# Kernel optimization log

Hardware: AMD Instinct MI355X
Metric: run time of the kernel (lower is better)

Reference implementation:

```python
import jax, jax.numpy as jnp
import numpy as np

N_NODES = 8192
IN_DIM = 20000
HID = 256
LAT = 64
N_EDGES = 262144


def setup_inputs() -> dict:
    key = jax.random.key(0)
    ks = jax.random.split(key, 12)
    s_in = 1.0 / np.sqrt(IN_DIM)
    s_h = 1.0 / np.sqrt(HID)
    s_l = 1.0 / np.sqrt(LAT)
    return {
        "x": jax.random.normal(ks[0], (N_NODES, IN_DIM), jnp.float32),
        "edge_index": jax.random.randint(ks[1], (2, N_EDGES), 0, N_NODES, jnp.int64 if jax.config.jax_enable_x64 else jnp.int32),
        "w_gcn": jax.random.uniform(ks[2], (IN_DIM, HID), jnp.float32, -s_in, s_in),
        "b_gcn": jnp.zeros((HID,), jnp.float32),
        "w_enc": jax.random.uniform(ks[3], (HID, LAT), jnp.float32, -s_h, s_h),
        "b_enc": jax.random.uniform(ks[4], (LAT,), jnp.float32, -s_h, s_h),
        "w_d1": jax.random.uniform(ks[5], (LAT, HID), jnp.float32, -s_l, s_l),
        "b_d1": jax.random.uniform(ks[6], (HID,), jnp.float32, -s_l, s_l),
        "w_d2": jax.random.uniform(ks[7], (HID, IN_DIM), jnp.float32, -s_h, s_h),
        "b_d2": jax.random.uniform(ks[8], (IN_DIM,), jnp.float32, -s_h, s_h),
    }


def _gcn_conv(x, edge_index, w, b):
    """PyG GCNConv (add_self_loops=True, normalize=True): A_hat @ (x W) + b."""
    n = x.shape[0]
    h = x @ w  # [N, HID] -- project first (in_dim >> out_dim)
    loops = jnp.arange(n, dtype=edge_index.dtype)
    row = jnp.concatenate([edge_index[0], loops])  # source nodes
    col = jnp.concatenate([edge_index[1], loops])  # target nodes
    deg = jax.ops.segment_sum(jnp.ones_like(col, dtype=h.dtype), col, num_segments=n)
    dinv = jnp.where(deg > 0, jax.lax.rsqrt(deg), 0.0)
    norm = dinv[row] * dinv[col]  # [E+N]
    msg = h[row] * norm[:, None]  # gather + scale
    out = jax.ops.segment_sum(msg, col, num_segments=n)  # scatter-add
    return out + b


def reference(x, edge_index, w_gcn, b_gcn, w_enc, b_enc, w_d1, b_d1, w_d2, b_d2):
    # Encoder: GCNConv -> ReLU -> (Dropout: eval no-op) -> Linear
    h = _gcn_conv(x, edge_index, w_gcn, b_gcn)
    latent = jax.nn.relu(h) @ w_enc + b_enc  # [N, LAT]
    # Decoder: Linear -> ReLU -> (Dropout) -> Linear
    recon = jax.nn.relu(latent @ w_d1 + b_d1) @ w_d2 + b_d2  # [N, IN_DIM]
    return recon, latent
```

## Files before the change

kernel.cpp:

```cpp
#include <hip/hip_runtime.h>
#include <stdint.h>

typedef short short8 __attribute__((ext_vector_type(8)));
typedef float f32x4 __attribute__((ext_vector_type(4)));

#define N_NODES 8192
#define IN_DIM 20000
#define HIDDEN 256
#define LATENT 64
#define N_EDGES 262144
#define K_STEPS 625
#define RECON_ELEMS (8192LL * 20000LL)
#define WD2T_ROWS 20096
#define NSUB3 626

static __device__ __forceinline__ unsigned short f2bf(float f) {
  union { float f; unsigned int u; } v;
  v.f = f;
  unsigned int u = v.u;
  return (unsigned short)((u + 0x7FFFu + ((u >> 16) & 1u)) >> 16);
}

static __device__ __forceinline__ unsigned pk2bf(float a, float b) {
  return (unsigned)f2bf(a) | ((unsigned)f2bf(b) << 16);
}

__global__ void k_count(const int* __restrict__ col, int* __restrict__ cnt) {
  int e = blockIdx.x * 256 + threadIdx.x;
  if (e < N_EDGES) atomicAdd(&cnt[col[e]], 1);
}

__global__ void k_dinv(const int* __restrict__ cnt, float* __restrict__ dinv) {
  int i = blockIdx.x * 256 + threadIdx.x;
  if (i < N_NODES) dinv[i] = rsqrtf((float)(cnt[i] + 1));
}

__global__ void k_scan(const int* __restrict__ cnt, int* __restrict__ offs,
                       int* __restrict__ cursor) {
  __shared__ int ps[256];
  int t = threadIdx.x;
  int local[32];
  int s = 0;
#pragma unroll
  for (int i = 0; i < 32; ++i) { local[i] = cnt[t * 32 + i]; s += local[i]; }
  ps[t] = s;
  __syncthreads();
  for (int d = 1; d < 256; d <<= 1) {
    int v = (t >= d) ? ps[t - d] : 0;
    __syncthreads();
    ps[t] += v;
    __syncthreads();
  }
  int pre = (t == 0) ? 0 : ps[t - 1];
#pragma unroll
  for (int i = 0; i < 32; ++i) {
    offs[t * 32 + i] = pre;
    cursor[t * 32 + i] = pre;
    pre += local[i];
  }
  if (t == 255) offs[N_NODES] = pre;
}

__global__ void k_fill(const int* __restrict__ row, const int* __restrict__ col,
                       int* __restrict__ cursor, int* __restrict__ csr_src) {
  int e = blockIdx.x * 256 + threadIdx.x;
  if (e < N_EDGES) {
    int c = col[e];
    int pos = atomicAdd(&cursor[c], 1);
    csr_src[pos] = row[e];
  }
}

__global__ void k_pack_wgcn(const float* __restrict__ w, unsigned short* __restrict__ pk) {
  int s = blockIdx.x;
  int t = threadIdx.x;
  int k0 = s * 32;
  unsigned int packed[16];
#pragma unroll
  for (int j = 0; j < 16; ++j) {
    float a = w[(size_t)(k0 + 2 * j) * HIDDEN + t];
    float b = w[(size_t)(k0 + 2 * j + 1) * HIDDEN + t];
    packed[j] = pk2bf(a, b);
  }
  uint4* dst = (uint4*)(pk + ((size_t)s * HIDDEN + t) * 32);
#pragma unroll
  for (int j = 0; j < 4; ++j)
    dst[j] = make_uint4(packed[4 * j], packed[4 * j + 1], packed[4 * j + 2], packed[4 * j + 3]);
}

__global__ void k_twd2(const float* __restrict__ wd2, unsigned short* __restrict__ wd2t) {
  __shared__ float tile[HIDDEN * 64];
  int n0 = blockIdx.x * 64;
  int t = threadIdx.x;
  int tk = t >> 6;
  int tn = t & 63;
#pragma unroll 4
  for (int kb = 0; kb < 64; ++kb) {
    int k = kb * 4 + tk;
    int n = n0 + tn;
    tile[k * 64 + tn] = (n < IN_DIM) ? wd2[(size_t)k * IN_DIM + n] : 0.0f;
  }
  __syncthreads();
  int rl = t >> 2;
  int q = t & 3;
  unsigned int packed[32];
#pragma unroll
  for (int j = 0; j < 32; ++j) {
    float a = tile[(q * 64 + 2 * j) * 64 + rl];
    float b = tile[(q * 64 + 2 * j + 1) * 64 + rl];
    packed[j] = pk2bf(a, b);
  }
  int rs = rl & 7;
  uint4* dst = (uint4*)(wd2t + (size_t)(n0 + rl) * HIDDEN + q * 64);
#pragma unroll
  for (int j = 0; j < 8; ++j)
    dst[j ^ rs] = make_uint4(packed[4 * j], packed[4 * j + 1], packed[4 * j + 2], packed[4 * j + 3]);
}

__global__ __launch_bounds__(256, 4)
void k_gemm1(const float* __restrict__ x, const unsigned short* __restrict__ wpk,
             float* __restrict__ h0p) {
  const int wgid = blockIdx.x;
  const int xcd = wgid & 7;
  const int split = xcd >> 1;
  const int m0 = (((wgid >> 3) << 1) | (xcd & 1)) << 5;
  const int s_beg = split * 156;

  const int t = threadIdx.x;
  const int lane = t & 63;
  const int wn = t >> 6;
  const int lr = lane & 15;
  const int lg = lane >> 4;

  __shared__ unsigned short Al[2][32 * 128];

  const int r = t >> 3;
  const int c8 = t & 7;
  const float* ap = x + (size_t)(m0 + r) * IN_DIM + s_beg * 32 + c8 * 4;

  auto wrA = [&](int buf, const float4* u) {
#pragma unroll
    for (int j = 0; j < 4; ++j) {
      int cc = (c8 >> 1) + j * 4;
      int idx = r * 128 + (((cc + r) & 15) << 3) + ((c8 & 1) << 2);
      *(uint2*)&Al[buf][idx] = make_uint2(pk2bf(u[j].x, u[j].y), pk2bf(u[j].z, u[j].w));
    }
  };

  const unsigned short* bq = wpk + ((size_t)s_beg * HIDDEN + wn * 64 + lr) * 32 + lg * 8;

  f32x4 acc[2][4];
#pragma unroll
  for (int i = 0; i < 2; ++i)
#pragma unroll
    for (int j = 0; j < 4; ++j) acc[i][j] = (f32x4){0.f, 0.f, 0.f, 0.f};

  {
    float4 u[4];
#pragma unroll
    for (int j = 0; j < 4; ++j) u[j] = *(const float4*)(ap + j * 32);
    wrA(0, u);
  }
  __syncthreads();

  int cur = 0;
  for (int mi = 0; mi < 39; ++mi) {
    float4 v[4];
    if (mi < 38) {
#pragma unroll
      for (int j = 0; j < 4; ++j)
        v[j] = *(const float4*)(ap + (mi + 1) * 128 + j * 32);
    }
#pragma unroll
    for (int ks = 0; ks < 4; ++ks) {
      short8 b0 = *(const short8*)(bq);
      short8 b1 = *(const short8*)(bq + 512);
      short8 b2 = *(const short8*)(bq + 1024);
      short8 b3 = *(const short8*)(bq + 1536);
      const int cra = (((ks * 4 + lg) + lr) & 15) << 3;
      short8 a0 = *(const short8*)&Al[cur][lr * 128 + cra];
      short8 a1 = *(const short8*)&Al[cur][(16 + lr) * 128 + cra];
      acc[0][0] = __builtin_amdgcn_mfma_f32_16x16x32_bf16(a0, b0, acc[0][0], 0, 0, 0);
      acc[1][0] = __builtin_amdgcn_mfma_f32_16x16x32_bf16(a1, b0, acc[1][0], 0, 0, 0);
      acc[0][1] = __builtin_amdgcn_mfma_f32_16x16x32_bf16(a0, b1, acc[0][1], 0, 0, 0);
      acc[1][1] = __builtin_amdgcn_mfma_f32_16x16x32_bf16(a1, b1, acc[1][1], 0, 0, 0);
      acc[0][2] = __builtin_amdgcn_mfma_f32_16x16x32_bf16(a0, b2, acc[0][2], 0, 0, 0);
      acc[1][2] = __builtin_amdgcn_mfma_f32_16x16x32_bf16(a1, b2, acc[1][2], 0, 0, 0);
      acc[0][3] = __builtin_amdgcn_mfma_f32_16x16x32_bf16(a0, b3, acc[0][3], 0, 0, 0);
      acc[1][3] = __builtin_amdgcn_mfma_f32_16x16x32_bf16(a1, b3, acc[1][3], 0, 0, 0);
      bq += HIDDEN * 32;
    }
    __syncthreads();
    if (mi < 38) wrA(cur ^ 1, v);
    __syncthreads();
    cur ^= 1;
  }

  if (split == 3) {
    const float* a0p = x + (size_t)(m0 + lr) * IN_DIM + 624 * 32 + lg * 8;
    const float* a1p = x + (size_t)(m0 + 16 + lr) * IN_DIM + 624 * 32 + lg * 8;
    float4 w0 = *(const float4*)a0p, w1 = *(const float4*)(a0p + 4);
    float4 w2 = *(const float4*)a1p, w3 = *(const float4*)(a1p + 4);
    uint4 af0 = make_uint4(pk2bf(w0.x, w0.y), pk2bf(w0.z, w0.w), pk2bf(w1.x, w1.y), pk2bf(w1.z, w1.w));
    uint4 af1 = make_uint4(pk2bf(w2.x, w2.y), pk2bf(w2.z, w2.w), pk2bf(w3.x, w3.y), pk2bf(w3.z, w3.w));
    short8 a0 = *(short8*)&af0;
    short8 a1 = *(short8*)&af1;
    short8 b0 = *(const short8*)(bq);
    short8 b1 = *(const short8*)(bq + 512);
    short8 b2 = *(const short8*)(bq + 1024);
    short8 b3 = *(const short8*)(bq + 1536);
    acc[0][0] = __builtin_amdgcn_mfma_f32_16x16x32_bf16(a0, b0, acc[0][0], 0, 0, 0);
    acc[1][0] = __builtin_amdgcn_mfma_f32_16x16x32_bf16(a1, b0, acc[1][0], 0, 0, 0);
    acc[0][1] = __builtin_amdgcn_mfma_f32_16x16x32_bf16(a0, b1, acc[0][1], 0, 0, 0);
    acc[1][1] = __builtin_amdgcn_mfma_f32_16x16x32_bf16(a1, b1, acc[1][1], 0, 0, 0);
    acc[0][2] = __builtin_amdgcn_mfma_f32_16x16x32_bf16(a0, b2, acc[0][2], 0, 0, 0);
    acc[1][2] = __builtin_amdgcn_mfma_f32_16x16x32_bf16(a1, b2, acc[1][2], 0, 0, 0);
    acc[0][3] = __builtin_amdgcn_mfma_f32_16x16x32_bf16(a0, b3, acc[0][3], 0, 0, 0);
    acc[1][3] = __builtin_amdgcn_mfma_f32_16x16x32_bf16(a1, b3, acc[1][3], 0, 0, 0);
  }

  float* outp = h0p + (size_t)split * (N_NODES * HIDDEN) + (size_t)m0 * HIDDEN;
#pragma unroll
  for (int mt = 0; mt < 2; ++mt)
#pragma unroll
    for (int nt = 0; nt < 4; ++nt) {
      int col = wn * 64 + nt * 16 + lr;
#pragma unroll
      for (int rr = 0; rr < 4; ++rr) {
        int rowi = mt * 16 + lg * 4 + rr;
        outp[rowi * HIDDEN + col] = acc[mt][nt][rr];
      }
    }
}

__global__ void k_sum(const float* __restrict__ p, float* __restrict__ h0) {
  int i = blockIdx.x * 256 + threadIdx.x;
  float4 a = ((const float4*)p)[i];
  float4 b = ((const float4*)p)[i + (N_NODES * HIDDEN / 4)];
  float4 c = ((const float4*)p)[i + 2 * (N_NODES * HIDDEN / 4)];
  float4 d = ((const float4*)p)[i + 3 * (N_NODES * HIDDEN / 4)];
  float4 r;
  r.x = (a.x + b.x) + (c.x + d.x);
  r.y = (a.y + b.y) + (c.y + d.y);
  r.z = (a.z + b.z) + (c.z + d.z);
  r.w = (a.w + b.w) + (c.w + d.w);
  ((float4*)h0)[i] = r;
}

__global__ void k_agg(const float* __restrict__ h0, const float* __restrict__ dinv,
                      const int* __restrict__ offs, const int* __restrict__ csr_src,
                      const float* __restrict__ bias, float* __restrict__ hrelu) {
  int c = blockIdx.x;
  int t = threadIdx.x;
  float dc = dinv[c];
  float acc = h0[(size_t)c * HIDDEN + t] * dc * dc;
  int beg = offs[c], end = offs[c + 1];
  for (int i = beg; i < end; ++i) {
    int r = csr_src[i];
    float wgt = dinv[r] * dc;
    acc += h0[(size_t)r * HIDDEN + t] * wgt;
  }
  float v = acc + bias[t];
  hrelu[(size_t)c * HIDDEN + t] = v > 0.f ? v : 0.f;
}

__global__ void k_enc(const float* __restrict__ hrelu, const float* __restrict__ w_enc,
                      const float* __restrict__ b_enc, float* __restrict__ latent) {
  __shared__ float hrow[4 * HIDDEN];
  int nb = blockIdx.x * 4;
  int t = threadIdx.x;
#pragma unroll
  for (int j = 0; j < 4; ++j) hrow[j * HIDDEN + t] = hrelu[(size_t)(nb + j) * HIDDEN + t];
  __syncthreads();
  int lat = t & 63;
  int nl = t >> 6;
  float acc = b_enc[lat];
#pragma unroll 8
  for (int k = 0; k < HIDDEN; ++k)
    acc += hrow[nl * HIDDEN + k] * w_enc[k * LATENT + lat];
  latent[(size_t)(nb + nl) * LATENT + lat] = acc;
}

__global__ void k_dec1(const float* __restrict__ latent, const float* __restrict__ w_d1,
                       const float* __restrict__ b_d1, unsigned short* __restrict__ hid2) {
  __shared__ float lrow[4 * LATENT];
  int nb = blockIdx.x * 4;
  int t = threadIdx.x;
  lrow[t] = latent[(size_t)nb * LATENT + t];
  __syncthreads();
  float b = b_d1[t];
  float a0 = b, a1 = b, a2 = b, a3 = b;
#pragma unroll 8
  for (int k = 0; k < LATENT; ++k) {
    float wv = w_d1[k * HIDDEN + t];
    a0 += lrow[k] * wv;
    a1 += lrow[LATENT + k] * wv;
    a2 += lrow[2 * LATENT + k] * wv;
    a3 += lrow[3 * LATENT + k] * wv;
  }
  hid2[(size_t)nb * HIDDEN + t]       = f2bf(a0 > 0.f ? a0 : 0.f);
  hid2[(size_t)(nb + 1) * HIDDEN + t] = f2bf(a1 > 0.f ? a1 : 0.f);
  hid2[(size_t)(nb + 2) * HIDDEN + t] = f2bf(a2 > 0.f ? a2 : 0.f);
  hid2[(size_t)(nb + 3) * HIDDEN + t] = f2bf(a3 > 0.f ? a3 : 0.f);
}

__global__ __launch_bounds__(256, 4)
void k_gemm3(const unsigned short* __restrict__ hid2, const unsigned short* __restrict__ wd2t,
             const float* __restrict__ b_d2, float* __restrict__ recon) {
  __shared__ unsigned short Bl[2][32 * 256];
  __shared__ float TB[4 * 512];
  const int wgid = blockIdx.x;
  const int chunk = ((wgid & 7) << 1) | (wgid >> 9);
  const int m0 = ((wgid >> 3) & 63) * 128;
  const int t = threadIdx.x;
  const int lane = t & 63;
  const int wid = t >> 6;
  const int lr = lane & 15;
  const int lg = lane >> 4;
  const int s0 = (NSUB3 * chunk) >> 4;
  const int s1 = (NSUB3 * (chunk + 1)) >> 4;

  short8 a[2][8];
#pragma unroll
  for (int mt = 0; mt < 2; ++mt)
#pragma unroll
    for (int ks = 0; ks < 8; ++ks)
      a[mt][ks] = *(const short8*)(hid2 + (size_t)(m0 + wid * 32 + mt * 16 + lr) * 256 + ks * 32 + lg * 8);

  auto stage = [&](int sub, int buf) {
#pragma unroll
    for (int i = 0; i < 4; ++i) {
      const unsigned short* g = wd2t + (size_t)sub * (32 * 256) + ((wid * 4 + i) * 512 + lane * 8);
      unsigned short* l = &Bl[buf][(wid * 4 + i) * 512];
      __builtin_amdgcn_global_load_lds(
          (const __attribute__((address_space(1))) unsigned int*)g,
          (__attribute__((address_space(3))) unsigned int*)l, 16, 0, 0);
    }
  };

  stage(s0, 0);
  __syncthreads();

  int cur = 0;
  for (int sub = s0; sub < s1; ++sub) {
    if (sub + 1 < s1) stage(sub + 1, cur ^ 1);

    f32x4 acc[2][2];
#pragma unroll
    for (int i = 0; i < 2; ++i) {
      acc[i][0] = (f32x4){0.f, 0.f, 0.f, 0.f};
      acc[i][1] = (f32x4){0.f, 0.f, 0.f, 0.f};
    }

    const int rl0 = lr;
    const int rl1 = 16 + lr;
#pragma unroll
    for (int ks = 0; ks < 8; ++ks) {
      short8 b0 = *(const short8*)&Bl[cur][rl0 * 256 + (((ks * 4 + lg) ^ (rl0 & 7)) << 3)];
      short8 b1 = *(const short8*)&Bl[cur][rl1 * 256 + (((ks * 4 + lg) ^ (rl1 & 7)) << 3)];
#pragma unroll
      for (int mt = 0; mt < 2; ++mt) {
        acc[mt][0] = __builtin_amdgcn_mfma_f32_16x16x32_bf16(a[mt][ks], b0, acc[mt][0], 0, 0, 0);
        acc[mt][1] = __builtin_amdgcn_mfma_f32_16x16x32_bf16(a[mt][ks], b1, acc[mt][1], 0, 0, 0);
      }
    }

    const int cg = (lane & 7) * 4;
    const int gc = sub * 32 + cg;
    f32x4 bias4 = (f32x4){0.f, 0.f, 0.f, 0.f};
    if (gc < IN_DIM) bias4 = *(const f32x4*)&b_d2[gc];
    float* TBw = TB + wid * 512;
#pragma unroll
    for (int mt = 0; mt < 2; ++mt) {
#pragma unroll
      for (int nt = 0; nt < 2; ++nt)
#pragma unroll
        for (int rr = 0; rr < 4; ++rr) {
          int row = lg * 4 + rr;
          TBw[row * 32 + ((nt * 16 + lr) ^ (((row >> 2) & 1) << 4))] = acc[mt][nt][rr];
        }
#pragma unroll
      for (int p = 0; p < 2; ++p) {
        int row = p * 8 + (lane >> 3);
        f32x4 v = *(const f32x4*)&TB[wid * 512 + row * 32 + (cg ^ (((row >> 2) & 1) << 4))];
        if (gc < IN_DIM) {
          int gr = m0 + wid * 32 + mt * 16 + row;
          *(f32x4*)&recon[(size_t)gr * IN_DIM + gc] = v + bias4;
        }
      }
    }
    __syncthreads();
    cur ^= 1;
  }
}

extern "C" void kernel_launch(void* const* d_in, const int* in_sizes, int n_in,
                              void* d_out, int out_size, void* d_ws, size_t ws_size,
                              hipStream_t stream) {
  const float* x     = (const float*)d_in[0];
  const int*   edge  = (const int*)d_in[1];
  const float* w_gcn = (const float*)d_in[2];
  const float* b_gcn = (const float*)d_in[3];
  const float* w_enc = (const float*)d_in[4];
  const float* b_enc = (const float*)d_in[5];
  const float* w_d1  = (const float*)d_in[6];
  const float* b_d1  = (const float*)d_in[7];
  const float* w_d2  = (const float*)d_in[8];
  const float* b_d2  = (const float*)d_in[9];
  float* out = (float*)d_out;
  (void)in_sizes; (void)n_in; (void)out_size; (void)ws_size;

  char* ws = (char*)d_ws;
  size_t o = 0;
  auto alloc = [&](size_t bytes) {
    char* p = ws + o;
    o += (bytes + 255) & ~(size_t)255;
    return p;
  };
  unsigned short* wpk  = (unsigned short*)alloc((size_t)K_STEPS * HIDDEN * 32 * 2);
  unsigned short* wd2t = (unsigned short*)alloc((size_t)WD2T_ROWS * HIDDEN * 2);
  float* h0p  = (float*)alloc((size_t)4 * N_NODES * HIDDEN * 4);
  float* h0   = (float*)alloc((size_t)N_NODES * HIDDEN * 4);
  float* hrel = (float*)alloc((size_t)N_NODES * HIDDEN * 4);
  unsigned short* hid2 = (unsigned short*)alloc((size_t)N_NODES * HIDDEN * 2);
  int* cnt    = (int*)alloc(N_NODES * 4);
  float* dinv = (float*)alloc(N_NODES * 4);
  int* offs   = (int*)alloc((N_NODES + 1) * 4);
  int* cursor = (int*)alloc(N_NODES * 4);
  int* csr    = (int*)alloc((size_t)N_EDGES * 4);

  const int* erow = edge;
  const int* ecol = edge + N_EDGES;

  hipMemsetAsync(cnt, 0, N_NODES * 4, stream);
  k_count<<<N_EDGES / 256, 256, 0, stream>>>(ecol, cnt);
  k_scan<<<1, 256, 0, stream>>>(cnt, offs, cursor);
  k_dinv<<<N_NODES / 256, 256, 0, stream>>>(cnt, dinv);
  k_fill<<<N_EDGES / 256, 256, 0, stream>>>(erow, ecol, cursor, csr);
  k_pack_wgcn<<<K_STEPS, 256, 0, stream>>>(w_gcn, wpk);
  k_twd2<<<WD2T_ROWS / 64, 256, 0, stream>>>(w_d2, wd2t);
  k_gemm1<<<1024, 256, 0, stream>>>(x, wpk, h0p);
  k_sum<<<(N_NODES * HIDDEN / 4) / 256, 256, 0, stream>>>(h0p, h0);
  k_agg<<<N_NODES, 256, 0, stream>>>(h0, dinv, offs, csr, b_gcn, hrel);
  float* latent = out + RECON_ELEMS;
  k_enc<<<N_NODES / 4, 256, 0, stream>>>(hrel, w_enc, b_enc, latent);
  k_dec1<<<N_NODES / 4, 256, 0, stream>>>(latent, w_d1, b_d1, hid2);
  k_gemm3<<<1024, 256, 0, stream>>>(hid2, wd2t, b_d2, out);
}
```

Before: 635.7 us.

## Restructure decoder GEMM to keep weight panels resident and widen GEMM1 K-tiles

```diff
diff --git a/kernel.cpp b/kernel.cpp
--- a/kernel.cpp
+++ b/kernel.cpp
@@ -12,7 +12,7 @@
 #define K_STEPS 625
 #define RECON_ELEMS (8192LL * 20000LL)
 #define WD2T_ROWS 20096
-#define NSUB3 626
+#define PANELS 157
 
 static __device__ __forceinline__ unsigned short f2bf(float f) {
   union { float f; unsigned int u; } v;
@@ -124,30 +124,32 @@
   const int xcd = wgid & 7;
   const int split = xcd >> 1;
   const int m0 = (((wgid >> 3) << 1) | (xcd & 1)) << 5;
-  const int s_beg = split * 156;
+  const int mac_beg = (split == 0) ? 0 : (split == 1) ? 20 : (split == 2) ? 40 : 59;
+  const int mac_end = (split == 0) ? 20 : (split == 1) ? 40 : (split == 2) ? 59 : 78;
+  const int s_beg_k = mac_beg * 8;
+  const int NM = mac_end - mac_beg;
 
   const int t = threadIdx.x;
   const int lane = t & 63;
-  const int wn = t >> 6;
+  const int w = t >> 6;
   const int lr = lane & 15;
   const int lg = lane >> 4;
 
-  __shared__ unsigned short Al[2][32 * 128];
-
-  const int r = t >> 3;
-  const int c8 = t & 7;
-  const float* ap = x + (size_t)(m0 + r) * IN_DIM + s_beg * 32 + c8 * 4;
-
-  auto wrA = [&](int buf, const float4* u) {
-#pragma unroll
-    for (int j = 0; j < 4; ++j) {
-      int cc = (c8 >> 1) + j * 4;
-      int idx = r * 128 + (((cc + r) & 15) << 3) + ((c8 & 1) << 2);
-      *(uint2*)&Al[buf][idx] = make_uint2(pk2bf(u[j].x, u[j].y), pk2bf(u[j].z, u[j].w));
+  __shared__ unsigned short Al[2][32 * 256];
+
+  const float* xbase = x + (size_t)(m0 + w * 8) * IN_DIM + (size_t)s_beg_k * 32 + lane * 4;
+
+  auto wrA = [&](int buf, const float4* v) {
+#pragma unroll
+    for (int i = 0; i < 8; ++i) {
+      int rloc = w * 8 + i;
+      int cc = (lane >> 1) ^ rloc;
+      *(uint2*)&Al[buf][rloc * 256 + cc * 8 + (lane & 1) * 4] =
+          make_uint2(pk2bf(v[i].x, v[i].y), pk2bf(v[i].z, v[i].w));
     }
   };
 
-  const unsigned short* bq = wpk + ((size_t)s_beg * HIDDEN + wn * 64 + lr) * 32 + lg * 8;
+  const unsigned short* bq = wpk + ((size_t)s_beg_k * HIDDEN + w * 64 + lr) * 32 + lg * 8;
 
   f32x4 acc[2][4];
 #pragma unroll
@@ -155,31 +157,29 @@
 #pragma unroll
     for (int j = 0; j < 4; ++j) acc[i][j] = (f32x4){0.f, 0.f, 0.f, 0.f};
 
-  {
-    float4 u[4];
-#pragma unroll
-    for (int j = 0; j < 4; ++j) u[j] = *(const float4*)(ap + j * 32);
-    wrA(0, u);
-  }
+  float4 v[8];
+#pragma unroll
+  for (int i = 0; i < 8; ++i) v[i] = *(const float4*)(xbase + (size_t)i * IN_DIM);
+  wrA(0, v);
   __syncthreads();
 
   int cur = 0;
-  for (int mi = 0; mi < 39; ++mi) {
-    float4 v[4];
-    if (mi < 38) {
-#pragma unroll
-      for (int j = 0; j < 4; ++j)
-        v[j] = *(const float4*)(ap + (mi + 1) * 128 + j * 32);
-    }
-#pragma unroll
-    for (int ks = 0; ks < 4; ++ks) {
+  for (int mi = 0; mi < NM; ++mi) {
+    const bool more = (mi + 1 < NM);
+    if (more) {
+#pragma unroll
+      for (int i = 0; i < 8; ++i)
+        v[i] = *(const float4*)(xbase + (size_t)(mi + 1) * 256 + (size_t)i * IN_DIM);
+    }
+#pragma unroll
+    for (int ks = 0; ks < 8; ++ks) {
       short8 b0 = *(const short8*)(bq);
       short8 b1 = *(const short8*)(bq + 512);
       short8 b2 = *(const short8*)(bq + 1024);
       short8 b3 = *(const short8*)(bq + 1536);
-      const int cra = (((ks * 4 + lg) + lr) & 15) << 3;
-      short8 a0 = *(const short8*)&Al[cur][lr * 128 + cra];
-      short8 a1 = *(const short8*)&Al[cur][(16 + lr) * 128 + cra];
+      const int c0 = ks * 4 + lg;
+      short8 a0 = *(const short8*)&Al[cur][lr * 256 + ((c0 ^ lr) << 3)];
+      short8 a1 = *(const short8*)&Al[cur][(16 + lr) * 256 + ((c0 ^ (16 + lr)) << 3)];
       acc[0][0] = __builtin_amdgcn_mfma_f32_16x16x32_bf16(a0, b0, acc[0][0], 0, 0, 0);
       acc[1][0] = __builtin_amdgcn_mfma_f32_16x16x32_bf16(a1, b0, acc[1][0], 0, 0, 0);
       acc[0][1] = __builtin_amdgcn_mfma_f32_16x16x32_bf16(a0, b1, acc[0][1], 0, 0, 0);
@@ -191,8 +191,10 @@
       bq += HIDDEN * 32;
     }
     __syncthreads();
-    if (mi < 38) wrA(cur ^ 1, v);
-    __syncthreads();
+    if (more) {
+      wrA(cur ^ 1, v);
+      __syncthreads();
+    }
     cur ^= 1;
   }
 
@@ -224,7 +226,7 @@
   for (int mt = 0; mt < 2; ++mt)
 #pragma unroll
     for (int nt = 0; nt < 4; ++nt) {
-      int col = wn * 64 + nt * 16 + lr;
+      int col = w * 64 + nt * 16 + lr;
 #pragma unroll
       for (int rr = 0; rr < 4; ++rr) {
         int rowi = mt * 16 + lg * 4 + rr;
@@ -304,46 +306,43 @@
   hid2[(size_t)(nb + 3) * HIDDEN + t] = f2bf(a3 > 0.f ? a3 : 0.f);
 }
 
-__global__ __launch_bounds__(256, 4)
+__global__ __launch_bounds__(256, 2)
 void k_gemm3(const unsigned short* __restrict__ hid2, const unsigned short* __restrict__ wd2t,
              const float* __restrict__ b_d2, float* __restrict__ recon) {
-  __shared__ unsigned short Bl[2][32 * 256];
-  __shared__ float TB[4 * 512];
-  const int wgid = blockIdx.x;
-  const int chunk = ((wgid & 7) << 1) | (wgid >> 9);
-  const int m0 = ((wgid >> 3) & 63) * 128;
+  __shared__ unsigned short Bp[128 * 256];
+  __shared__ float TB[32 * 128];
+  const int rc = blockIdx.x;
+  const int pn = blockIdx.y;
+  const int n0 = pn * 128;
+  const int r0 = rc * 1024;
   const int t = threadIdx.x;
   const int lane = t & 63;
-  const int wid = t >> 6;
+  const int w = t >> 6;
   const int lr = lane & 15;
   const int lg = lane >> 4;
-  const int s0 = (NSUB3 * chunk) >> 4;
-  const int s1 = (NSUB3 * (chunk + 1)) >> 4;
-
-  short8 a[2][8];
-#pragma unroll
-  for (int mt = 0; mt < 2; ++mt)
-#pragma unroll
-    for (int ks = 0; ks < 8; ++ks)
-      a[mt][ks] = *(const short8*)(hid2 + (size_t)(m0 + wid * 32 + mt * 16 + lr) * 256 + ks * 32 + lg * 8);
-
-  auto stage = [&](int sub, int buf) {
-#pragma unroll
-    for (int i = 0; i < 4; ++i) {
-      const unsigned short* g = wd2t + (size_t)sub * (32 * 256) + ((wid * 4 + i) * 512 + lane * 8);
-      unsigned short* l = &Bl[buf][(wid * 4 + i) * 512];
-      __builtin_amdgcn_global_load_lds(
-          (const __attribute__((address_space(1))) unsigned int*)g,
-          (__attribute__((address_space(3))) unsigned int*)l, 16, 0, 0);
-    }
-  };
-
-  stage(s0, 0);
-  __syncthreads();
-
-  int cur = 0;
-  for (int sub = s0; sub < s1; ++sub) {
-    if (sub + 1 < s1) stage(sub + 1, cur ^ 1);
+
+#pragma unroll
+  for (int i = 0; i < 16; ++i) {
+    int seg = w * 16 + i;
+    __builtin_amdgcn_global_load_lds(
+        (const __attribute__((address_space(1))) unsigned int*)(wd2t + (size_t)n0 * 256 + seg * 512 + lane * 8),
+        (__attribute__((address_space(3))) unsigned int*)(Bp + seg * 512), 16, 0, 0);
+  }
+
+  const int col4 = (t & 31) * 4;
+  const int gc = n0 + col4;
+  f32x4 bias4 = (f32x4){0.f, 0.f, 0.f, 0.f};
+  if (gc < IN_DIM) bias4 = *(const f32x4*)&b_d2[gc];
+  __syncthreads();
+
+  for (int st = 0; st < 32; ++st) {
+    const int rs = r0 + st * 32;
+    short8 a[2][8];
+#pragma unroll
+    for (int mt = 0; mt < 2; ++mt)
+#pragma unroll
+      for (int ks = 0; ks < 8; ++ks)
+        a[mt][ks] = *(const short8*)(hid2 + (size_t)(rs + mt * 16 + lr) * 256 + ks * 32 + lg * 8);
 
     f32x4 acc[2][2];
 #pragma unroll
@@ -351,13 +350,12 @@
       acc[i][0] = (f32x4){0.f, 0.f, 0.f, 0.f};
       acc[i][1] = (f32x4){0.f, 0.f, 0.f, 0.f};
     }
-
-    const int rl0 = lr;
-    const int rl1 = 16 + lr;
+    const int nl0 = w * 32 + lr;
+    const int nl1 = nl0 + 16;
 #pragma unroll
     for (int ks = 0; ks < 8; ++ks) {
-      short8 b0 = *(const short8*)&Bl[cur][rl0 * 256 + (((ks * 4 + lg) ^ (rl0 & 7)) << 3)];
-      short8 b1 = *(const short8*)&Bl[cur][rl1 * 256 + (((ks * 4 + lg) ^ (rl1 & 7)) << 3)];
+      short8 b0 = *(const short8*)&Bp[nl0 * 256 + (((ks * 4 + lg) ^ (nl0 & 7)) << 3)];
+      short8 b1 = *(const short8*)&Bp[nl1 * 256 + (((ks * 4 + lg) ^ (nl1 & 7)) << 3)];
 #pragma unroll
       for (int mt = 0; mt < 2; ++mt) {
         acc[mt][0] = __builtin_amdgcn_mfma_f32_16x16x32_bf16(a[mt][ks], b0, acc[mt][0], 0, 0, 0);
@@ -365,32 +363,27 @@
       }
     }
 
-    const int cg = (lane & 7) * 4;
-    const int gc = sub * 32 + cg;
-    f32x4 bias4 = (f32x4){0.f, 0.f, 0.f, 0.f};
-    if (gc < IN_DIM) bias4 = *(const f32x4*)&b_d2[gc];
-    float* TBw = TB + wid * 512;
-#pragma unroll
-    for (int mt = 0; mt < 2; ++mt) {
+#pragma unroll
+    for (int mt = 0; mt < 2; ++mt)
 #pragma unroll
       for (int nt = 0; nt < 2; ++nt)
 #pragma unroll
         for (int rr = 0; rr < 4; ++rr) {
-          int row = lg * 4 + rr;
-          TBw[row * 32 + ((nt * 16 + lr) ^ (((row >> 2) & 1) << 4))] = acc[mt][nt][rr];
+          int row = mt * 16 + lg * 4 + rr;
+          int col = w * 32 + nt * 16 + lr;
+          TB[row * 128 + col] = acc[mt][nt][rr];
         }
-#pragma unroll
-      for (int p = 0; p < 2; ++p) {
-        int row = p * 8 + (lane >> 3);
-        f32x4 v = *(const f32x4*)&TB[wid * 512 + row * 32 + (cg ^ (((row >> 2) & 1) << 4))];
-        if (gc < IN_DIM) {
-          int gr = m0 + wid * 32 + mt * 16 + row;
-          *(f32x4*)&recon[(size_t)gr * IN_DIM + gc] = v + bias4;
-        }
+    __syncthreads();
+
+    if (gc < IN_DIM) {
+#pragma unroll
+      for (int sw = 0; sw < 4; ++sw) {
+        int row = sw * 8 + (t >> 5);
+        f32x4 v = *(const f32x4*)&TB[row * 128 + col4];
+        *(f32x4*)&recon[(size_t)(rs + row) * IN_DIM + gc] = v + bias4;
       }
     }
     __syncthreads();
-    cur ^= 1;
   }
 }
 
@@ -445,5 +438,5 @@
   float* latent = out + RECON_ELEMS;
   k_enc<<<N_NODES / 4, 256, 0, stream>>>(hrel, w_enc, b_enc, latent);
   k_dec1<<<N_NODES / 4, 256, 0, stream>>>(latent, w_d1, b_d1, hid2);
-  k_gemm3<<<1024, 256, 0, stream>>>(hid2, wd2t, b_d2, out);
-}
+  k_gemm3<<<dim3(8, PANELS), 256, 0, stream>>>(hid2, wd2t, b_d2, out);
+}
```

Measured after the change: 970.0 us. 52.6% more time.

## Batch four column subtiles per epilogue in decoder GEMM for wider stores

Applied to the files above, without the earlier changes.

```diff
diff --git a/kernel.cpp b/kernel.cpp
--- a/kernel.cpp
+++ b/kernel.cpp
@@ -11,8 +11,8 @@
 #define N_EDGES 262144
 #define K_STEPS 625
 #define RECON_ELEMS (8192LL * 20000LL)
-#define WD2T_ROWS 20096
-#define NSUB3 626
+#define WD2T_ROWS 20480
+#define NSUB3 640
 
 static __device__ __forceinline__ unsigned short f2bf(float f) {
   union { float f; unsigned int u; } v;
@@ -191,8 +191,10 @@
       bq += HIDDEN * 32;
     }
     __syncthreads();
-    if (mi < 38) wrA(cur ^ 1, v);
-    __syncthreads();
+    if (mi < 38) {
+      wrA(cur ^ 1, v);
+      __syncthreads();
+    }
     cur ^= 1;
   }
 
@@ -304,11 +306,11 @@
   hid2[(size_t)(nb + 3) * HIDDEN + t] = f2bf(a3 > 0.f ? a3 : 0.f);
 }
 
-__global__ __launch_bounds__(256, 4)
+__global__ __launch_bounds__(256, 3)
 void k_gemm3(const unsigned short* __restrict__ hid2, const unsigned short* __restrict__ wd2t,
              const float* __restrict__ b_d2, float* __restrict__ recon) {
   __shared__ unsigned short Bl[2][32 * 256];
-  __shared__ float TB[4 * 512];
+  __shared__ float TB[4][8 * 132];
   const int wgid = blockIdx.x;
   const int chunk = ((wgid & 7) << 1) | (wgid >> 9);
   const int m0 = ((wgid >> 3) & 63) * 128;
@@ -317,8 +319,8 @@
   const int wid = t >> 6;
   const int lr = lane & 15;
   const int lg = lane >> 4;
-  const int s0 = (NSUB3 * chunk) >> 4;
-  const int s1 = (NSUB3 * (chunk + 1)) >> 4;
+  const int s0 = chunk * 40;
+  const int s1 = s0 + 40;
 
   short8 a[2][8];
 #pragma unroll
@@ -342,55 +344,66 @@
   __syncthreads();
 
   int cur = 0;
-  for (int sub = s0; sub < s1; ++sub) {
-    if (sub + 1 < s1) stage(sub + 1, cur ^ 1);
-
-    f32x4 acc[2][2];
-#pragma unroll
-    for (int i = 0; i < 2; ++i) {
-      acc[i][0] = (f32x4){0.f, 0.f, 0.f, 0.f};
-      acc[i][1] = (f32x4){0.f, 0.f, 0.f, 0.f};
-    }
-
-    const int rl0 = lr;
-    const int rl1 = 16 + lr;
-#pragma unroll
-    for (int ks = 0; ks < 8; ++ks) {
-      short8 b0 = *(const short8*)&Bl[cur][rl0 * 256 + (((ks * 4 + lg) ^ (rl0 & 7)) << 3)];
-      short8 b1 = *(const short8*)&Bl[cur][rl1 * 256 + (((ks * 4 + lg) ^ (rl1 & 7)) << 3)];
+  for (int sb = 0; sb < 10; ++sb) {
+    const int sub0 = s0 + sb * 4;
+
+    f32x4 acc4[4][2][2];
+#pragma unroll
+    for (int bi = 0; bi < 4; ++bi)
 #pragma unroll
       for (int mt = 0; mt < 2; ++mt) {
-        acc[mt][0] = __builtin_amdgcn_mfma_f32_16x16x32_bf16(a[mt][ks], b0, acc[mt][0], 0, 0, 0);
-        acc[mt][1] = __builtin_amdgcn_mfma_f32_16x16x32_bf16(a[mt][ks], b1, acc[mt][1], 0, 0, 0);
+        acc4[bi][mt][0] = (f32x4){0.f, 0.f, 0.f, 0.f};
+        acc4[bi][mt][1] = (f32x4){0.f, 0.f, 0.f, 0.f};
       }
-    }
-
-    const int cg = (lane & 7) * 4;
-    const int gc = sub * 32 + cg;
-    f32x4 bias4 = (f32x4){0.f, 0.f, 0.f, 0.f};
-    if (gc < IN_DIM) bias4 = *(const f32x4*)&b_d2[gc];
-    float* TBw = TB + wid * 512;
-#pragma unroll
-    for (int mt = 0; mt < 2; ++mt) {
-#pragma unroll
-      for (int nt = 0; nt < 2; ++nt)
-#pragma unroll
-        for (int rr = 0; rr < 4; ++rr) {
-          int row = lg * 4 + rr;
-          TBw[row * 32 + ((nt * 16 + lr) ^ (((row >> 2) & 1) << 4))] = acc[mt][nt][rr];
-        }
-#pragma unroll
-      for (int p = 0; p < 2; ++p) {
-        int row = p * 8 + (lane >> 3);
-        f32x4 v = *(const f32x4*)&TB[wid * 512 + row * 32 + (cg ^ (((row >> 2) & 1) << 4))];
-        if (gc < IN_DIM) {
-          int gr = m0 + wid * 32 + mt * 16 + row;
-          *(f32x4*)&recon[(size_t)gr * IN_DIM + gc] = v + bias4;
+
+#pragma unroll
+    for (int bi = 0; bi < 4; ++bi) {
+      const int sub = sub0 + bi;
+      if (sub + 1 < s1) stage(sub + 1, cur ^ 1);
+      const int rl0 = lr;
+      const int rl1 = 16 + lr;
+#pragma unroll
+      for (int ks = 0; ks < 8; ++ks) {
+        short8 b0 = *(const short8*)&Bl[cur][rl0 * 256 + (((ks * 4 + lg) ^ (rl0 & 7)) << 3)];
+        short8 b1 = *(const short8*)&Bl[cur][rl1 * 256 + (((ks * 4 + lg) ^ (rl1 & 7)) << 3)];
+#pragma unroll
+        for (int mt = 0; mt < 2; ++mt) {
+          acc4[bi][mt][0] = __builtin_amdgcn_mfma_f32_16x16x32_bf16(a[mt][ks], b0, acc4[bi][mt][0], 0, 0, 0);
+          acc4[bi][mt][1] = __builtin_amdgcn_mfma_f32_16x16x32_bf16(a[mt][ks], b1, acc4[bi][mt][1], 0, 0, 0);
         }
       }
-    }
-    __syncthreads();
-    cur ^= 1;
+      __syncthreads();
+      cur ^= 1;
+    }
+
+    const int cbase = sub0 * 32;
+    const int gcol = cbase + (lane & 31) * 4;
+    f32x4 bias4 = (f32x4){0.f, 0.f, 0.f, 0.f};
+    if (gcol < IN_DIM) bias4 = *(const f32x4*)&b_d2[gcol];
+    float* TBw = TB[wid];
+#pragma unroll
+    for (int p = 0; p < 4; ++p) {
+      const int mt = p >> 1;
+      if ((lg >> 1) == (p & 1)) {
+        const int r8 = (lg & 1) * 4;
+#pragma unroll
+        for (int bi = 0; bi < 4; ++bi)
+#pragma unroll
+          for (int nt = 0; nt < 2; ++nt)
+#pragma unroll
+            for (int rr = 0; rr < 4; ++rr)
+              TBw[(r8 + rr) * 132 + bi * 32 + nt * 16 + lr] = acc4[bi][mt][nt][rr];
+      }
+#pragma unroll
+      for (int q = 0; q < 4; ++q) {
+        const int r8 = q * 2 + (lane >> 5);
+        f32x4 v = *(const f32x4*)&TBw[r8 * 132 + (lane & 31) * 4];
+        if (gcol < IN_DIM) {
+          const int gr = m0 + wid * 32 + p * 8 + r8;
+          *(f32x4*)&recon[(size_t)gr * IN_DIM + gcol] = v + bias4;
+        }
+      }
+    }
   }
 }
 
```

After: 749.1 us. +17.8%, slower.

## Widen GEMM1 K-tile to 512 with row-contiguous x loads and rebalanced splits

Applied to the files above, without the earlier changes.

```diff
diff --git a/kernel.cpp b/kernel.cpp
--- a/kernel.cpp
+++ b/kernel.cpp
@@ -117,37 +117,41 @@
     dst[j ^ rs] = make_uint4(packed[4 * j], packed[4 * j + 1], packed[4 * j + 2], packed[4 * j + 3]);
 }
 
-__global__ __launch_bounds__(256, 4)
+__global__ __launch_bounds__(256, 2)
 void k_gemm1(const float* __restrict__ x, const unsigned short* __restrict__ wpk,
              float* __restrict__ h0p) {
   const int wgid = blockIdx.x;
   const int xcd = wgid & 7;
   const int split = xcd >> 1;
   const int m0 = (((wgid >> 3) << 1) | (xcd & 1)) << 5;
-  const int s_beg = split * 156;
+  const int NM = (split == 3) ? 9 : 10;
+  const int s_beg_k = split * 160;
 
   const int t = threadIdx.x;
   const int lane = t & 63;
-  const int wn = t >> 6;
+  const int w = t >> 6;
   const int lr = lane & 15;
   const int lg = lane >> 4;
 
-  __shared__ unsigned short Al[2][32 * 128];
-
-  const int r = t >> 3;
-  const int c8 = t & 7;
-  const float* ap = x + (size_t)(m0 + r) * IN_DIM + s_beg * 32 + c8 * 4;
-
-  auto wrA = [&](int buf, const float4* u) {
-#pragma unroll
-    for (int j = 0; j < 4; ++j) {
-      int cc = (c8 >> 1) + j * 4;
-      int idx = r * 128 + (((cc + r) & 15) << 3) + ((c8 & 1) << 2);
-      *(uint2*)&Al[buf][idx] = make_uint2(pk2bf(u[j].x, u[j].y), pk2bf(u[j].z, u[j].w));
+  __shared__ unsigned short Al[2][32 * 512];
+
+  const float* xbase = x + (size_t)(m0 + w * 8) * IN_DIM + s_beg_k * 32 + lane * 4;
+
+  auto wrA = [&](int buf, float4 (*v)[2]) {
+#pragma unroll
+    for (int i = 0; i < 8; ++i) {
+      int row = w * 8 + i;
+#pragma unroll
+      for (int j = 0; j < 2; ++j) {
+        int c = (j * 32 + (lane >> 1)) ^ row;
+        int idx = row * 512 + c * 8 + (lane & 1) * 4;
+        *(uint2*)&Al[buf][idx] = make_uint2(pk2bf(v[i][j].x, v[i][j].y),
+                                            pk2bf(v[i][j].z, v[i][j].w));
+      }
     }
   };
 
-  const unsigned short* bq = wpk + ((size_t)s_beg * HIDDEN + wn * 64 + lr) * 32 + lg * 8;
+  const unsigned short* bq = wpk + ((size_t)s_beg_k * HIDDEN + w * 64 + lr) * 32 + lg * 8;
 
   f32x4 acc[2][4];
 #pragma unroll
@@ -155,31 +159,36 @@
 #pragma unroll
     for (int j = 0; j < 4; ++j) acc[i][j] = (f32x4){0.f, 0.f, 0.f, 0.f};
 
+  float4 v[8][2];
   {
-    float4 u[4];
-#pragma unroll
-    for (int j = 0; j < 4; ++j) u[j] = *(const float4*)(ap + j * 32);
-    wrA(0, u);
+#pragma unroll
+    for (int i = 0; i < 8; ++i) {
+      v[i][0] = *(const float4*)(xbase + (size_t)i * IN_DIM);
+      v[i][1] = *(const float4*)(xbase + (size_t)i * IN_DIM + 256);
+    }
+    wrA(0, v);
   }
   __syncthreads();
 
   int cur = 0;
-  for (int mi = 0; mi < 39; ++mi) {
-    float4 v[4];
-    if (mi < 38) {
-#pragma unroll
-      for (int j = 0; j < 4; ++j)
-        v[j] = *(const float4*)(ap + (mi + 1) * 128 + j * 32);
-    }
-#pragma unroll
-    for (int ks = 0; ks < 4; ++ks) {
+  for (int mi = 0; mi < NM; ++mi) {
+    const bool more = (mi + 1 < NM);
+    if (more) {
+#pragma unroll
+      for (int i = 0; i < 8; ++i) {
+        v[i][0] = *(const float4*)(xbase + (size_t)(mi + 1) * 512 + (size_t)i * IN_DIM);
+        v[i][1] = *(const float4*)(xbase + (size_t)(mi + 1) * 512 + (size_t)i * IN_DIM + 256);
+      }
+    }
+#pragma unroll
+    for (int ks = 0; ks < 16; ++ks) {
       short8 b0 = *(const short8*)(bq);
       short8 b1 = *(const short8*)(bq + 512);
       short8 b2 = *(const short8*)(bq + 1024);
       short8 b3 = *(const short8*)(bq + 1536);
-      const int cra = (((ks * 4 + lg) + lr) & 15) << 3;
-      short8 a0 = *(const short8*)&Al[cur][lr * 128 + cra];
-      short8 a1 = *(const short8*)&Al[cur][(16 + lr) * 128 + cra];
+      const int c0 = 4 * ks + lg;
+      short8 a0 = *(const short8*)&Al[cur][lr * 512 + ((c0 ^ lr) << 3)];
+      short8 a1 = *(const short8*)&Al[cur][(16 + lr) * 512 + ((c0 ^ (16 + lr)) << 3)];
       acc[0][0] = __builtin_amdgcn_mfma_f32_16x16x32_bf16(a0, b0, acc[0][0], 0, 0, 0);
       acc[1][0] = __builtin_amdgcn_mfma_f32_16x16x32_bf16(a1, b0, acc[1][0], 0, 0, 0);
       acc[0][1] = __builtin_amdgcn_mfma_f32_16x16x32_bf16(a0, b1, acc[0][1], 0, 0, 0);
@@ -191,8 +200,10 @@
       bq += HIDDEN * 32;
     }
     __syncthreads();
-    if (mi < 38) wrA(cur ^ 1, v);
-    __syncthreads();
+    if (more) {
+      wrA(cur ^ 1, v);
+      __syncthreads();
+    }
     cur ^= 1;
   }
 
@@ -224,7 +235,7 @@
   for (int mt = 0; mt < 2; ++mt)
 #pragma unroll
     for (int nt = 0; nt < 4; ++nt) {
-      int col = wn * 64 + nt * 16 + lr;
+      int col = w * 64 + nt * 16 + lr;
 #pragma unroll
       for (int rr = 0; rr < 4; ++rr) {
         int rowi = mt * 16 + lg * 4 + rr;
@@ -304,7 +315,7 @@
   hid2[(size_t)(nb + 3) * HIDDEN + t] = f2bf(a3 > 0.f ? a3 : 0.f);
 }
 
-__global__ __launch_bounds__(256, 4)
+__global__ __launch_bounds__(256, 2)
 void k_gemm3(const unsigned short* __restrict__ hid2, const unsigned short* __restrict__ wd2t,
              const float* __restrict__ b_d2, float* __restrict__ recon) {
   __shared__ unsigned short Bl[2][32 * 256];
```

Measured after the change: 680.6 us. +7.1%, slower.
